# Kernel optimization log

Hardware: AMD Instinct MI355X
Metric: run time of the kernel (lower is better)

## Reference

```python
import jax, jax.numpy as jnp
import numpy as np

B, N, D = 2, 2048, 768
H = 12
HD = D // H  # 64

def setup_inputs() -> dict:
    key = jax.random.key(0)
    ks = jax.random.split(key, 5)
    scale = 1.0 / np.sqrt(D)
    return {
        "x": jax.random.normal(ks[0], (B, N, D), dtype=jnp.float32),
        "W_kqv": jax.random.normal(ks[1], (H, 3 * HD, D), dtype=jnp.float32) * scale,
        "b_kqv": jax.random.normal(ks[2], (H, 3 * HD), dtype=jnp.float32) * 0.01,
        "W_proj": jax.random.normal(ks[3], (D, D), dtype=jnp.float32) * scale,
        "b_proj": jax.random.normal(ks[4], (D,), dtype=jnp.float32) * 0.01,
    }

def reference(x, W_kqv, b_kqv, W_proj, b_proj):
    # Per-head Linear: x @ W_h^T + b_h, all heads at once -> [B, H, N, 3*HD]
    kqv = jnp.einsum('bnd,hod->bhno', x, W_kqv) + b_kqv[None, :, None, :]
    k, q, v = jnp.split(kqv, 3, axis=-1)  # each [B, H, N, HD]
    # scores = q @ k^T / sqrt(head_dim)  (attention_scores(a=k, b=q))
    scores = jnp.einsum('bhqd,bhkd->bhqk', q, k) / jnp.sqrt(jnp.asarray(HD, x.dtype))
    # causal mask (tril): masked_fill with -inf where mask == 0
    causal = jnp.tril(jnp.ones((N, N), dtype=bool))
    scores = jnp.where(causal[None, None, :, :], scores, -jnp.inf)
    attn = jax.nn.softmax(scores, axis=-1)
    sa = jnp.einsum('bhqk,bhkd->bhqd', attn, v)  # [B, H, N, HD]
    # concat heads along feature dim (head order preserved)
    sa = sa.transpose(0, 2, 1, 3).reshape(B, N, D)
    # output projection
    return sa @ W_proj.T + b_proj
```

## Files before the change

kernel.cpp:

```cpp
#include <hip/hip_runtime.h>

#define BB 2
#define SEQ 2048
#define DIM 768
#define NH 12
#define HD 64

typedef _Float16 half8 __attribute__((ext_vector_type(8)));
typedef _Float16 half4 __attribute__((ext_vector_type(4)));
typedef float floatx4 __attribute__((ext_vector_type(4)));

__device__ __forceinline__ void gl_lds16(const _Float16* g, _Float16* l) {
    __builtin_amdgcn_global_load_lds(
        (const __attribute__((address_space(1))) void*)g,
        (__attribute__((address_space(3))) void*)l, 16, 0, 0);
}

__global__ __launch_bounds__(256)
void cvt3(const float* __restrict__ s0, _Float16* __restrict__ d0, int nb0,
          const float* __restrict__ s1, _Float16* __restrict__ d1, int nb1,
          const float* __restrict__ s2, _Float16* __restrict__ d2) {
    int b = blockIdx.x;
    const float* s; _Float16* d;
    if (b < nb0)            { s = s0; d = d0; }
    else if (b < nb0 + nb1) { s = s1; d = d1; b -= nb0; }
    else                    { s = s2; d = d2; b -= nb0 + nb1; }
    const int i = (b * 256 + threadIdx.x) * 8;
    float4 a = *(const float4*)(s + i);
    float4 c = *(const float4*)(s + i + 4);
    half8 h;
    h[0] = (_Float16)a.x; h[1] = (_Float16)a.y; h[2] = (_Float16)a.z; h[3] = (_Float16)a.w;
    h[4] = (_Float16)c.x; h[5] = (_Float16)c.y; h[6] = (_Float16)c.z; h[7] = (_Float16)c.w;
    *(half8*)(d + i) = h;
}

#define GEMM_CORE(APTR, BPTR)                                                   \
    __shared__ _Float16 Asl[2][128 * 32];                                       \
    __shared__ _Float16 Bsl[2][128 * 32];                                       \
    const int t = threadIdx.x, w = t >> 6, lane = t & 63;                       \
    const int quad = lane >> 4, l15 = lane & 15;                                \
    const int wm = w >> 1, wn = w & 1;                                          \
    const int m0 = blockIdx.y * 128, c0 = blockIdx.x * 128;                     \
    const floatx4 z4 = {0.f, 0.f, 0.f, 0.f};                                    \
    floatx4 acc[4][4];                                                          \
    _Pragma("unroll") for (int i = 0; i < 4; ++i)                               \
        _Pragma("unroll") for (int j = 0; j < 4; ++j) acc[i][j] = z4;           \
    const _Float16* pA = APTR + (size_t)(m0 + w * 32 + l15) * DIM + quad * 8;   \
    const _Float16* pB = BPTR + (size_t)(c0 + w * 32 + l15) * DIM + quad * 8;   \
    gl_lds16(pA,            &Asl[0][(w * 2 + 0) * 512]);                        \
    gl_lds16(pA + 16 * DIM, &Asl[0][(w * 2 + 1) * 512]);                        \
    gl_lds16(pB,            &Bsl[0][(w * 2 + 0) * 512]);                        \
    gl_lds16(pB + 16 * DIM, &Bsl[0][(w * 2 + 1) * 512]);                        \
    for (int k0 = 0, it = 0; k0 < DIM; k0 += 32, ++it) {                        \
        const int buf = it & 1;                                                 \
        __syncthreads();                                                        \
        if (k0 + 32 < DIM) {                                                    \
            gl_lds16(pA + k0 + 32,            &Asl[buf ^ 1][(w * 2 + 0) * 512]);\
            gl_lds16(pA + k0 + 32 + 16 * DIM, &Asl[buf ^ 1][(w * 2 + 1) * 512]);\
            gl_lds16(pB + k0 + 32,            &Bsl[buf ^ 1][(w * 2 + 0) * 512]);\
            gl_lds16(pB + k0 + 32 + 16 * DIM, &Bsl[buf ^ 1][(w * 2 + 1) * 512]);\
        }                                                                       \
        half8 af[4], bf[4];                                                     \
        _Pragma("unroll") for (int i = 0; i < 4; ++i)                           \
            af[i] = *(const half8*)&Asl[buf][(wm * 4 + i) * 512 + lane * 8];    \
        _Pragma("unroll") for (int j = 0; j < 4; ++j)                           \
            bf[j] = *(const half8*)&Bsl[buf][(wn * 4 + j) * 512 + lane * 8];    \
        _Pragma("unroll") for (int i = 0; i < 4; ++i)                           \
            _Pragma("unroll") for (int j = 0; j < 4; ++j)                       \
                acc[i][j] = __builtin_amdgcn_mfma_f32_16x16x32_f16(             \
                    af[i], bf[j], acc[i][j], 0, 0, 0);                          \
    }

__global__ __launch_bounds__(256)
void kqv_gemm2(const _Float16* __restrict__ xh, const _Float16* __restrict__ Wh,
               const float* __restrict__ bias, _Float16* __restrict__ kb,
               _Float16* __restrict__ qb, _Float16* __restrict__ vb) {
    GEMM_CORE(xh, Wh)
    #pragma unroll
    for (int j = 0; j < 4; ++j) {
        const int cbase = c0 + (wn * 4 + j) * 16;
        const int h = cbase / 192;
        const int rem = cbase - h * 192;
        const int part = rem >> 6;
        const int d = (rem & 63) + l15;
        _Float16* dst = (part == 0) ? kb : (part == 1 ? qb : vb);
        const float bv = bias[cbase + l15];
        #pragma unroll
        for (int i = 0; i < 4; ++i)
            #pragma unroll
            for (int r = 0; r < 4; ++r) {
                const int m = m0 + (wm * 4 + i) * 16 + quad * 4 + r;
                const int bidx = m >> 11, n = m & (SEQ - 1);
                dst[(((size_t)(bidx * NH + h) * SEQ + n) << 6) + d] =
                    (_Float16)(acc[i][j][r] + bv);
            }
    }
}

__global__ __launch_bounds__(256)
void proj_gemm3(const _Float16* __restrict__ A, const _Float16* __restrict__ Wh,
                const float* __restrict__ bias, float* __restrict__ out) {
    __shared__ _Float16 Asl[2][128 * 32];
    __shared__ _Float16 Bsl[2][64 * 32];
    const int t = threadIdx.x, w = t >> 6, lane = t & 63;
    const int quad = lane >> 4, l15 = lane & 15;
    const int wm = w >> 1, wn = w & 1;
    const int m0 = blockIdx.y * 128, c0 = blockIdx.x * 64;
    const floatx4 z4 = {0.f, 0.f, 0.f, 0.f};
    floatx4 acc[4][2];
    #pragma unroll
    for (int i = 0; i < 4; ++i)
        #pragma unroll
        for (int j = 0; j < 2; ++j) acc[i][j] = z4;
    const _Float16* pA = A  + (size_t)(m0 + w * 32 + l15) * DIM + quad * 8;
    const _Float16* pB = Wh + (size_t)(c0 + w * 16 + l15) * DIM + quad * 8;
    gl_lds16(pA,            &Asl[0][(w * 2 + 0) * 512]);
    gl_lds16(pA + 16 * DIM, &Asl[0][(w * 2 + 1) * 512]);
    gl_lds16(pB,            &Bsl[0][w * 512]);
    for (int k0 = 0, it = 0; k0 < DIM; k0 += 32, ++it) {
        const int buf = it & 1;
        __syncthreads();
        if (k0 + 32 < DIM) {
            gl_lds16(pA + k0 + 32,            &Asl[buf ^ 1][(w * 2 + 0) * 512]);
            gl_lds16(pA + k0 + 32 + 16 * DIM, &Asl[buf ^ 1][(w * 2 + 1) * 512]);
            gl_lds16(pB + k0 + 32,            &Bsl[buf ^ 1][w * 512]);
        }
        half8 af[4], bf[2];
        #pragma unroll
        for (int i = 0; i < 4; ++i)
            af[i] = *(const half8*)&Asl[buf][(wm * 4 + i) * 512 + lane * 8];
        #pragma unroll
        for (int j = 0; j < 2; ++j)
            bf[j] = *(const half8*)&Bsl[buf][(wn * 2 + j) * 512 + lane * 8];
        #pragma unroll
        for (int i = 0; i < 4; ++i)
            #pragma unroll
            for (int j = 0; j < 2; ++j)
                acc[i][j] = __builtin_amdgcn_mfma_f32_16x16x32_f16(
                    af[i], bf[j], acc[i][j], 0, 0, 0);
    }
    #pragma unroll
    for (int j = 0; j < 2; ++j) {
        const int cbase = c0 + (wn * 2 + j) * 16;
        const float bv = bias[cbase + l15];
        #pragma unroll
        for (int i = 0; i < 4; ++i)
            #pragma unroll
            for (int r = 0; r < 4; ++r) {
                const int m = m0 + (wm * 4 + i) * 16 + quad * 4 + r;
                out[(size_t)m * DIM + cbase + l15] = acc[i][j][r] + bv;
            }
    }
}

__global__ __launch_bounds__(256)
void v_transpose(const _Float16* __restrict__ vb, _Float16* __restrict__ vbT) {
    __shared__ _Float16 T[64 * 72];
    const int t = threadIdx.x;
    const int s0 = blockIdx.x * 64;
    const size_t base = (size_t)blockIdx.y * (SEQ * HD);
    {
        const int s = t >> 2, doff = (t & 3) * 16;
        const _Float16* src = vb + base + (size_t)(s0 + s) * HD + doff;
        *(half8*)&T[s * 72 + doff]     = *(const half8*)src;
        *(half8*)&T[s * 72 + doff + 8] = *(const half8*)(src + 8);
    }
    __syncthreads();
    {
        const int d = t >> 2, soff = (t & 3) * 16;
        half8 o0, o1;
        #pragma unroll
        for (int k = 0; k < 8; ++k) o0[k] = T[(soff + k) * 72 + d];
        #pragma unroll
        for (int k = 0; k < 8; ++k) o1[k] = T[(soff + 8 + k) * 72 + d];
        _Float16* dst = vbT + base + (size_t)d * SEQ + s0 + soff;
        *(half8*)dst       = o0;
        *(half8*)(dst + 8) = o1;
    }
}

__global__ __launch_bounds__(256)
void attn_mfma(const _Float16* __restrict__ qb, const _Float16* __restrict__ kbuf,
               const _Float16* __restrict__ vbT, _Float16* __restrict__ sa,
               _Float16* __restrict__ Opart, float* __restrict__ lpart) {
    __shared__ _Float16 Kl[2][64 * 64];
    __shared__ _Float16 Vl[2][64 * 64];
    __shared__ _Float16 Pl[4][16 * 64];
    int u = 39 - blockIdx.x, q, p, np;
    if (u < 4)       { q = u;               p = 0;     np = 1; }
    else if (u < 12) { int v = u - 4;  q = 4  + (v >> 1); p = v & 1; np = 2; }
    else if (u < 24) { int v = u - 12; q = 8  + v / 3;    p = v % 3; np = 3; }
    else             { int v = u - 24; q = 12 + (v >> 2); p = v & 3; np = 4; }
    const int ntiles = 2 * q + 2;
    const int kt0 = p * 8;
    const int ktn = (p == np - 1) ? (ntiles - kt0) : 8;

    const int bh = blockIdx.y;
    const int t = threadIdx.x, w = t >> 6, lane = t & 63, quad = lane >> 4, l15 = lane & 15;
    const size_t base = (size_t)bh * (SEQ * HD);
    const int i0 = q * 128 + w * 32;
    _Float16* Pw = Pl[w];
    const _Float16* Kg = kbuf + base;
    const _Float16* Vg = vbT + base;

    const int lr = lane >> 3, gg = lane & 7;
    const int gs = (gg ^ (lr & 7)) * 8;

    half8 aq[2][2];
    const _Float16 qs = (_Float16)(0.125f * 1.44269504f);
    #pragma unroll
    for (int rt = 0; rt < 2; ++rt)
        #pragma unroll
        for (int ks = 0; ks < 2; ++ks) {
            aq[rt][ks] = *(const half8*)(qb + base +
                          (size_t)(i0 + rt * 16 + l15) * HD + ks * 32 + quad * 8);
            #pragma unroll
            for (int k = 0; k < 8; ++k) aq[rt][ks][k] *= qs;
        }

    half8 ones;
    #pragma unroll
    for (int k = 0; k < 8; ++k) ones[k] = (_Float16)1.0f;

    const floatx4 z4 = {0.f, 0.f, 0.f, 0.f};
    floatx4 O[2][4], l_acc[2];
    #pragma unroll
    for (int rt = 0; rt < 2; ++rt) {
        l_acc[rt] = z4;
        #pragma unroll
        for (int k = 0; k < 4; ++k) O[rt][k] = z4;
    }

    #pragma unroll
    for (int pp = 0; pp < 2; ++pp) {
        const int c = w * 2 + pp, row = c * 8 + lr;
        gl_lds16(Kg + (size_t)(kt0 * 64 + row) * HD + gs,  &Kl[0][c * 512]);
        gl_lds16(Vg + (size_t)row * SEQ + kt0 * 64 + gs,   &Vl[0][c * 512]);
    }

    const int swz = l15 & 7;
    const int pmask = (l15 & 7) << 1;
    const int prbase = l15 * 64;

    for (int it = 0; it < ktn; ++it) {
        const int kt = kt0 + it;
        const int buf = it & 1;
        const int j0 = kt * 64;
        __syncthreads();

        if (it + 1 < ktn) {
            const _Float16* Kn = Kg + (size_t)(j0 + 64) * HD;
            const _Float16* Vn = Vg + (j0 + 64);
            #pragma unroll
            for (int pp = 0; pp < 2; ++pp) {
                const int c = w * 2 + pp, row = c * 8 + lr;
                gl_lds16(Kn + (size_t)row * HD + gs,  &Kl[buf ^ 1][c * 512]);
                gl_lds16(Vn + (size_t)row * SEQ + gs, &Vl[buf ^ 1][c * 512]);
            }
        }
        if (j0 > i0 + 31) continue;

        floatx4 S[2][4];
        #pragma unroll
        for (int rt = 0; rt < 2; ++rt)
            #pragma unroll
            for (int nt = 0; nt < 4; ++nt) S[rt][nt] = z4;
        #pragma unroll
        for (int ks = 0; ks < 2; ++ks)
            #pragma unroll
            for (int nt = 0; nt < 4; ++nt) {
                half8 bk = *(const half8*)&Kl[buf][(nt * 16 + l15) * 64 +
                                                   (((ks * 4 + quad) ^ swz) << 3)];
                S[0][nt] = __builtin_amdgcn_mfma_f32_16x16x32_f16(bk, aq[0][ks], S[0][nt], 0, 0, 0);
                S[1][nt] = __builtin_amdgcn_mfma_f32_16x16x32_f16(bk, aq[1][ks], S[1][nt], 0, 0, 0);
            }

        half8 bvr[2][4];
        #pragma unroll
        for (int ks = 0; ks < 2; ++ks)
            #pragma unroll
            for (int dt = 0; dt < 4; ++dt)
                bvr[ks][dt] = *(const half8*)&Vl[buf][(dt * 16 + l15) * 64 +
                                                      (((ks * 4 + quad) ^ swz) << 3)];

        const bool masked = (j0 + 63 > i0);
        #pragma unroll
        for (int rt = 0; rt < 2; ++rt) {
            asm volatile("" ::: "memory");
            const int iq = i0 + rt * 16 + l15;
            #pragma unroll
            for (int nt = 0; nt < 4; ++nt) {
                float pv[4];
                if (masked) {
                    const int jb = j0 + nt * 16 + quad * 4;
                    #pragma unroll
                    for (int r = 0; r < 4; ++r) {
                        float e = exp2f(S[rt][nt][r]);
                        pv[r] = (jb + r > iq) ? 0.f : e;
                    }
                } else {
                    #pragma unroll
                    for (int r = 0; r < 4; ++r) pv[r] = exp2f(S[rt][nt][r]);
                }
                auto lo = __builtin_amdgcn_cvt_pkrtz(pv[0], pv[1]);
                auto hi = __builtin_amdgcn_cvt_pkrtz(pv[2], pv[3]);
                half4 pk;
                pk[0] = (_Float16)lo[0]; pk[1] = (_Float16)lo[1];
                pk[2] = (_Float16)hi[0]; pk[3] = (_Float16)hi[1];
                const int slot = (nt * 4 + quad) ^ pmask;
                *(half4*)&Pw[prbase + slot * 4] = pk;
            }
            asm volatile("" ::: "memory");
            #pragma unroll
            for (int ks = 0; ks < 2; ++ks) {
                const int rslot = (ks * 8 + quad * 2) ^ pmask;
                half8 ap = *(const half8*)&Pw[prbase + rslot * 4];
                #pragma unroll
                for (int dt = 0; dt < 4; ++dt)
                    O[rt][dt] = __builtin_amdgcn_mfma_f32_16x16x32_f16(
                        ap, bvr[ks][dt], O[rt][dt], 0, 0, 0);
                l_acc[rt] = __builtin_amdgcn_mfma_f32_16x16x32_f16(
                    ap, ones, l_acc[rt], 0, 0, 0);
            }
        }
    }

    if (np == 1) {
        const int bidx = bh / NH, h = bh - bidx * NH;
        #pragma unroll
        for (int rt = 0; rt < 2; ++rt)
            #pragma unroll
            for (int r = 0; r < 4; ++r) {
                const float inv = 1.0f / l_acc[rt][r];
                const int i = i0 + rt * 16 + quad * 4 + r;
                #pragma unroll
                for (int dt = 0; dt < 4; ++dt)
                    sa[(size_t)(bidx * SEQ + i) * DIM + h * HD + dt * 16 + l15] =
                        (_Float16)(O[rt][dt][r] * inv);
            }
    } else {
        const size_t slot = ((size_t)(bh * 16 + q) * 4 + p);
        _Float16* Od = Opart + slot * 8192;
        float*    ld = lpart + slot * 128;
        #pragma unroll
        for (int rt = 0; rt < 2; ++rt)
            #pragma unroll
            for (int r = 0; r < 4; ++r) {
                const int row = w * 32 + rt * 16 + quad * 4 + r;
                ld[row] = l_acc[rt][r];
                #pragma unroll
                for (int dt = 0; dt < 4; ++dt)
                    Od[row * 64 + dt * 16 + l15] = (_Float16)O[rt][dt][r];
            }
    }
}

__global__ __launch_bounds__(256)
void attn_combine(const _Float16* __restrict__ Opart, const float* __restrict__ lpart,
                  _Float16* __restrict__ sa) {
    const int q = 4 + blockIdx.x;
    const int bh = blockIdx.y;
    const int np = (q < 8) ? 2 : (q < 12 ? 3 : 4);
    const int t = threadIdx.x;
    const int row = t >> 1, d0 = (t & 1) * 32;
    const size_t slot0 = (size_t)(bh * 16 + q) * 4;

    float lsum = 0.f;
    for (int p = 0; p < np; ++p) lsum += lpart[(slot0 + p) * 128 + row];

    float acc[32];
    #pragma unroll
    for (int k = 0; k < 32; ++k) acc[k] = 0.f;
    for (int p = 0; p < np; ++p) {
        const _Float16* src = Opart + (slot0 + p) * 8192 + row * 64 + d0;
        #pragma unroll
        for (int v = 0; v < 4; ++v) {
            half8 a = *(const half8*)(src + v * 8);
            #pragma unroll
            for (int k = 0; k < 8; ++k) acc[v * 8 + k] += (float)a[k];
        }
    }
    const float inv = 1.0f / lsum;
    const int bidx = bh / NH, h = bh - bidx * NH;
    _Float16* dst = sa + (size_t)(bidx * SEQ + q * 128 + row) * DIM + h * HD + d0;
    #pragma unroll
    for (int v = 0; v < 4; ++v) {
        half8 o;
        #pragma unroll
        for (int k = 0; k < 8; ++k) o[k] = (_Float16)(acc[v * 8 + k] * inv);
        *(half8*)(dst + v * 8) = o;
    }
}

extern "C" void kernel_launch(void* const* d_in, const int* in_sizes, int n_in,
                              void* d_out, int out_size, void* d_ws, size_t ws_size,
                              hipStream_t stream) {
    (void)in_sizes; (void)n_in; (void)out_size; (void)ws_size;
    const float* x  = (const float*)d_in[0];
    const float* Wk = (const float*)d_in[1];
    const float* bk = (const float*)d_in[2];
    const float* Wp = (const float*)d_in[3];
    const float* bp = (const float*)d_in[4];
    float* out = (float*)d_out;

    _Float16* ws = (_Float16*)d_ws;
    const size_t per = (size_t)BB * NH * SEQ * HD;
    const int nx = BB * SEQ * DIM;
    const int nwk = NH * 3 * HD * DIM;
    const int nwp = DIM * DIM;
    _Float16* kb  = ws;
    _Float16* qb  = ws + per;
    _Float16* vb  = ws + 2 * per;
    _Float16* vbT = ws + 3 * per;
    _Float16* sa  = ws + 4 * per;
    _Float16* xh  = ws + 5 * per;
    _Float16* Wkh = xh + nx;
    _Float16* Wph = Wkh + nwk;
    _Float16* Opart = Wph + nwp;
    float*    lpart = (float*)(Opart + (size_t)24 * 16 * 4 * 8192);

    const int nb0 = nx / 2048, nb1 = nwk / 2048, nb2 = nwp / 2048;
    cvt3<<<dim3(nb0 + nb1 + nb2), 256, 0, stream>>>(x, xh, nb0, Wk, Wkh, nb1, Wp, Wph);

    kqv_gemm2  <<<dim3(18, 32), 256, 0, stream>>>(xh, Wkh, bk, kb, qb, vb);
    v_transpose<<<dim3(32, 24), 256, 0, stream>>>(vb, vbT);
    attn_mfma  <<<dim3(40, 24), 256, 0, stream>>>(qb, kb, vbT, sa, Opart, lpart);
    attn_combine<<<dim3(12, 24), 256, 0, stream>>>(Opart, lpart, sa);
    proj_gemm3 <<<dim3(12, 32), 256, 0, stream>>>(sa, Wph, bp, out);
}
```

Measured before the change: 189.6 us.

## Fuse V transpose into QKV GEMM epilogue and split attention into finer chunks

The QKV GEMM epilogue now writes the V part straight into the transposed layout using packed half4 stores, which removes the separate v_transpose kernel and its extra pass over V. The attention split-K decomposition changes from up to 4 chunks of 8 key tiles to chunks of 4 key tiles, giving 72 blocks per head instead of 40. This is meant to balance the causal workload better across CUs. In exchange, more partial results go through the combine kernel and more workspace is used. The transposed V stores are strided by SEQ, so writes are less coalesced.

After: 187.5 us. No clear change (-1.1%).

```diff
diff --git a/kernel.cpp b/kernel.cpp
--- a/kernel.cpp
+++ b/kernel.cpp
@@ -74,7 +74,7 @@
 __global__ __launch_bounds__(256)
 void kqv_gemm2(const _Float16* __restrict__ xh, const _Float16* __restrict__ Wh,
                const float* __restrict__ bias, _Float16* __restrict__ kb,
-               _Float16* __restrict__ qb, _Float16* __restrict__ vb) {
+               _Float16* __restrict__ qb, _Float16* __restrict__ vbT) {
     GEMM_CORE(xh, Wh)
     #pragma unroll
     for (int j = 0; j < 4; ++j) {
@@ -83,17 +83,29 @@
         const int rem = cbase - h * 192;
         const int part = rem >> 6;
         const int d = (rem & 63) + l15;
-        _Float16* dst = (part == 0) ? kb : (part == 1 ? qb : vb);
         const float bv = bias[cbase + l15];
-        #pragma unroll
-        for (int i = 0; i < 4; ++i)
-            #pragma unroll
-            for (int r = 0; r < 4; ++r) {
-                const int m = m0 + (wm * 4 + i) * 16 + quad * 4 + r;
+        if (part == 2) {
+            #pragma unroll
+            for (int i = 0; i < 4; ++i) {
+                const int m = m0 + (wm * 4 + i) * 16 + quad * 4;
                 const int bidx = m >> 11, n = m & (SEQ - 1);
-                dst[(((size_t)(bidx * NH + h) * SEQ + n) << 6) + d] =
-                    (_Float16)(acc[i][j][r] + bv);
-            }
+                half4 pk;
+                #pragma unroll
+                for (int r = 0; r < 4; ++r) pk[r] = (_Float16)(acc[i][j][r] + bv);
+                *(half4*)(vbT + ((size_t)(bidx * NH + h) * HD + d) * SEQ + n) = pk;
+            }
+        } else {
+            _Float16* dst = (part == 0) ? kb : qb;
+            #pragma unroll
+            for (int i = 0; i < 4; ++i)
+                #pragma unroll
+                for (int r = 0; r < 4; ++r) {
+                    const int m = m0 + (wm * 4 + i) * 16 + quad * 4 + r;
+                    const int bidx = m >> 11, n = m & (SEQ - 1);
+                    dst[(((size_t)(bidx * NH + h) * SEQ + n) << 6) + d] =
+                        (_Float16)(acc[i][j][r] + bv);
+                }
+        }
     }
 }
 
@@ -154,46 +166,23 @@
 }
 
 __global__ __launch_bounds__(256)
-void v_transpose(const _Float16* __restrict__ vb, _Float16* __restrict__ vbT) {
-    __shared__ _Float16 T[64 * 72];
-    const int t = threadIdx.x;
-    const int s0 = blockIdx.x * 64;
-    const size_t base = (size_t)blockIdx.y * (SEQ * HD);
-    {
-        const int s = t >> 2, doff = (t & 3) * 16;
-        const _Float16* src = vb + base + (size_t)(s0 + s) * HD + doff;
-        *(half8*)&T[s * 72 + doff]     = *(const half8*)src;
-        *(half8*)&T[s * 72 + doff + 8] = *(const half8*)(src + 8);
-    }
-    __syncthreads();
-    {
-        const int d = t >> 2, soff = (t & 3) * 16;
-        half8 o0, o1;
-        #pragma unroll
-        for (int k = 0; k < 8; ++k) o0[k] = T[(soff + k) * 72 + d];
-        #pragma unroll
-        for (int k = 0; k < 8; ++k) o1[k] = T[(soff + 8 + k) * 72 + d];
-        _Float16* dst = vbT + base + (size_t)d * SEQ + s0 + soff;
-        *(half8*)dst       = o0;
-        *(half8*)(dst + 8) = o1;
-    }
-}
-
-__global__ __launch_bounds__(256)
 void attn_mfma(const _Float16* __restrict__ qb, const _Float16* __restrict__ kbuf,
                const _Float16* __restrict__ vbT, _Float16* __restrict__ sa,
                _Float16* __restrict__ Opart, float* __restrict__ lpart) {
     __shared__ _Float16 Kl[2][64 * 64];
     __shared__ _Float16 Vl[2][64 * 64];
     __shared__ _Float16 Pl[4][16 * 64];
-    int u = 39 - blockIdx.x, q, p, np;
-    if (u < 4)       { q = u;               p = 0;     np = 1; }
-    else if (u < 12) { int v = u - 4;  q = 4  + (v >> 1); p = v & 1; np = 2; }
-    else if (u < 24) { int v = u - 12; q = 8  + v / 3;    p = v % 3; np = 3; }
-    else             { int v = u - 24; q = 12 + (v >> 2); p = v & 3; np = 4; }
+    int u = 71 - blockIdx.x;
+    int k = 0;
+    while ((k + 1) * (k + 2) <= u) ++k;
+    const int rem = u - k * (k + 1);
+    const int hi = (rem >= (k + 1));
+    const int q = 2 * k + hi;
+    const int p = rem - (hi ? (k + 1) : 0);
     const int ntiles = 2 * q + 2;
-    const int kt0 = p * 8;
-    const int ktn = (p == np - 1) ? (ntiles - kt0) : 8;
+    const int kt0 = p * 4;
+    const int ktn = (ntiles - kt0 < 4) ? (ntiles - kt0) : 4;
+    const int np = (q + 2) >> 1;
 
     const int bh = blockIdx.y;
     const int t = threadIdx.x, w = t >> 6, lane = t & 63, quad = lane >> 4, l15 = lane & 15;
@@ -215,12 +204,12 @@
             aq[rt][ks] = *(const half8*)(qb + base +
                           (size_t)(i0 + rt * 16 + l15) * HD + ks * 32 + quad * 8);
             #pragma unroll
-            for (int k = 0; k < 8; ++k) aq[rt][ks][k] *= qs;
+            for (int kk = 0; kk < 8; ++kk) aq[rt][ks][kk] *= qs;
         }
 
     half8 ones;
     #pragma unroll
-    for (int k = 0; k < 8; ++k) ones[k] = (_Float16)1.0f;
+    for (int kk = 0; kk < 8; ++kk) ones[kk] = (_Float16)1.0f;
 
     const floatx4 z4 = {0.f, 0.f, 0.f, 0.f};
     floatx4 O[2][4], l_acc[2];
@@ -228,7 +217,7 @@
     for (int rt = 0; rt < 2; ++rt) {
         l_acc[rt] = z4;
         #pragma unroll
-        for (int k = 0; k < 4; ++k) O[rt][k] = z4;
+        for (int kk = 0; kk < 4; ++kk) O[rt][kk] = z4;
     }
 
     #pragma unroll
@@ -303,10 +292,10 @@
                     for (int r = 0; r < 4; ++r) pv[r] = exp2f(S[rt][nt][r]);
                 }
                 auto lo = __builtin_amdgcn_cvt_pkrtz(pv[0], pv[1]);
-                auto hi = __builtin_amdgcn_cvt_pkrtz(pv[2], pv[3]);
+                auto hi2 = __builtin_amdgcn_cvt_pkrtz(pv[2], pv[3]);
                 half4 pk;
                 pk[0] = (_Float16)lo[0]; pk[1] = (_Float16)lo[1];
-                pk[2] = (_Float16)hi[0]; pk[3] = (_Float16)hi[1];
+                pk[2] = (_Float16)hi2[0]; pk[3] = (_Float16)hi2[1];
                 const int slot = (nt * 4 + quad) ^ pmask;
                 *(half4*)&Pw[prbase + slot * 4] = pk;
             }
@@ -339,7 +328,7 @@
                         (_Float16)(O[rt][dt][r] * inv);
             }
     } else {
-        const size_t slot = ((size_t)(bh * 16 + q) * 4 + p);
+        const size_t slot = ((size_t)(bh * 16 + q) * 8 + p);
         _Float16* Od = Opart + slot * 8192;
         float*    ld = lpart + slot * 128;
         #pragma unroll
@@ -358,12 +347,12 @@
 __global__ __launch_bounds__(256)
 void attn_combine(const _Float16* __restrict__ Opart, const float* __restrict__ lpart,
                   _Float16* __restrict__ sa) {
-    const int q = 4 + blockIdx.x;
+    const int q = 2 + blockIdx.x;
     const int bh = blockIdx.y;
-    const int np = (q < 8) ? 2 : (q < 12 ? 3 : 4);
+    const int np = (q + 2) >> 1;
     const int t = threadIdx.x;
     const int row = t >> 1, d0 = (t & 1) * 32;
-    const size_t slot0 = (size_t)(bh * 16 + q) * 4;
+    const size_t slot0 = (size_t)(bh * 16 + q) * 8;
 
     float lsum = 0.f;
     for (int p = 0; p < np; ++p) lsum += lpart[(slot0 + p) * 128 + row];
@@ -410,21 +399,19 @@
     const int nwp = DIM * DIM;
     _Float16* kb  = ws;
     _Float16* qb  = ws + per;
-    _Float16* vb  = ws + 2 * per;
-    _Float16* vbT = ws + 3 * per;
-    _Float16* sa  = ws + 4 * per;
-    _Float16* xh  = ws + 5 * per;
+    _Float16* vbT = ws + 2 * per;
+    _Float16* sa  = ws + 3 * per;
+    _Float16* xh  = ws + 4 * per;
     _Float16* Wkh = xh + nx;
     _Float16* Wph = Wkh + nwk;
     _Float16* Opart = Wph + nwp;
-    float*    lpart = (float*)(Opart + (size_t)24 * 16 * 4 * 8192);
+    float*    lpart = (float*)(Opart + (size_t)24 * 16 * 8 * 8192);
 
     const int nb0 = nx / 2048, nb1 = nwk / 2048, nb2 = nwp / 2048;
     cvt3<<<dim3(nb0 + nb1 + nb2), 256, 0, stream>>>(x, xh, nb0, Wk, Wkh, nb1, Wp, Wph);
 
-    kqv_gemm2  <<<dim3(18, 32), 256, 0, stream>>>(xh, Wkh, bk, kb, qb, vb);
-    v_transpose<<<dim3(32, 24), 256, 0, stream>>>(vb, vbT);
-    attn_mfma  <<<dim3(40, 24), 256, 0, stream>>>(qb, kb, vbT, sa, Opart, lpart);
-    attn_combine<<<dim3(12, 24), 256, 0, stream>>>(Opart, lpart, sa);
+    kqv_gemm2  <<<dim3(18, 32), 256, 0, stream>>>(xh, Wkh, bk, kb, qb, vbT);
+    attn_mfma  <<<dim3(72, 24), 256, 0, stream>>>(qb, kb, vbT, sa, Opart, lpart);
+    attn_combine<<<dim3(14, 24), 256, 0, stream>>>(Opart, lpart, sa);
     proj_gemm3 <<<dim3(12, 32), 256, 0, stream>>>(sa, Wph, bp, out);
 }
```
